# Optimization experiments

Hardware: AMD Instinct MI355X
Metric: run time of the kernel (lower is better)

## Reference

```python
import jax, jax.numpy as jnp
import numpy as np

N = 50000      # num nodes
E = 800000     # num edges
F_IN = 100     # input features (ogbn-products)
HID = 128      # hidden_dim (per-head out_channels)
H = 2          # heads
OUT = 47       # num classes
NEG_SLOPE = 0.2


def setup_inputs() -> dict:
    key = jax.random.key(0)
    ks = jax.random.split(key, 14)
    def glorot(k, shape, fan):
        return jax.random.normal(k, shape, jnp.float32) * (1.0 / np.sqrt(fan))
    x = jax.random.normal(ks[0], (N, F_IN), jnp.float32)
    edge_index = jax.random.randint(ks[1], (2, E), 0, N)
    # GAT layer 0: lin_l (= lin_r, shared) weight [H*HID, F_IN], attention vecs [H, HID]
    W0 = glorot(ks[2], (H * HID, F_IN), F_IN)
    b0 = jnp.zeros((H * HID,), jnp.float32)
    attl0 = glorot(ks[3], (H, HID), HID)
    attr0 = glorot(ks[4], (H, HID), HID)
    # GAT layer 1: input dim H*HID
    W1 = glorot(ks[5], (H * HID, H * HID), H * HID)
    b1 = jnp.zeros((H * HID,), jnp.float32)
    attl1 = glorot(ks[6], (H, HID), HID)
    attr1 = glorot(ks[7], (H, HID), HID)
    # post_mp: Linear(H*HID -> HID), Linear(HID -> OUT)
    Wp1 = glorot(ks[8], (HID, H * HID), H * HID)
    bp1 = jnp.zeros((HID,), jnp.float32)
    Wp2 = glorot(ks[9], (OUT, HID), HID)
    bp2 = jnp.zeros((OUT,), jnp.float32)
    return dict(x=x, edge_index=edge_index, W0=W0, b0=b0, attl0=attl0, attr0=attr0,
                W1=W1, b1=b1, attl1=attl1, attr1=attr1,
                Wp1=Wp1, bp1=bp1, Wp2=Wp2, bp2=bp2)


def gat_layer(x, W, b, att_l, att_r, src, dst):
    # shared lin_l == lin_r in the source
    h = (x @ W.T + b).reshape(-1, H, HID)          # [N, H, C]
    alpha_l = jnp.einsum('nhc,hc->nh', h, att_l)   # per-node left scores
    alpha_r = jnp.einsum('nhc,hc->nh', h, att_r)   # per-node right scores
    e = jax.nn.leaky_relu(alpha_l[src] + alpha_r[dst], NEG_SLOPE)  # [E, H]
    # segment softmax over edges grouped by destination node
    emax = jax.ops.segment_max(e, dst, num_segments=N)             # [N, H]
    ee = jnp.exp(e - emax[dst])
    denom = jax.ops.segment_sum(ee, dst, num_segments=N)           # [N, H]
    a = ee / denom[dst]                                            # [E, H]
    msg = a[:, :, None] * h[src]                                   # [E, H, C]
    out = jax.ops.segment_sum(msg, dst, num_segments=N)            # [N, H, C]
    return out.reshape(-1, H * HID)


def reference(x, edge_index, W0, b0, attl0, attr0, W1, b1, attl1, attr1, Wp1, bp1, Wp2, bp2):
    src, dst = edge_index[0], edge_index[1]
    x = jax.nn.relu(gat_layer(x, W0, b0, attl0, attr0, src, dst))
    x = jax.nn.relu(gat_layer(x, W1, b1, attl1, attr1, src, dst))
    h = x @ Wp1.T + bp1           # dropout p=0.0 -> identity
    logits = h @ Wp2.T + bp2
    return jax.nn.log_softmax(logits, axis=1)
```

## Files before the change

### kernel.cpp

```cpp
#include <hip/hip_runtime.h>
#include <math.h>

#define N_NODES 50000
#define E_EDGES 800000
#define F_IN 100
#define HID 128
#define HEADS 2
#define OUT_C 47
#define HH (HEADS*HID)
#define MPAD 50048
#define SLOTS 64

typedef float floatx4 __attribute__((ext_vector_type(4)));
typedef float float2v __attribute__((ext_vector_type(2)));
typedef short short8 __attribute__((ext_vector_type(8)));

__device__ inline ushort bf16round(float v) {
    unsigned u = __float_as_uint(v);
    return (ushort)((u + 0x7FFFu + ((u >> 16) & 1u)) >> 16);
}

__device__ __forceinline__ void gl_lds16(const void* g, void* l) {
    __builtin_amdgcn_global_load_lds(
        (const __attribute__((address_space(1))) unsigned int*)g,
        (__attribute__((address_space(3))) unsigned int*)l, 16, 0, 0);
}

__device__ __forceinline__ void gemm_body(
    int bx, int by,
    const ushort* __restrict__ Ab, const ushort* __restrict__ Wb,
    const float* __restrict__ bias,
    ushort* __restrict__ Hb,
    const float* __restrict__ attl, const float* __restrict__ attr,
    float* __restrict__ al, float* __restrict__ ar,
    int M, int Kp, ushort* sA, ushort* sB)
{
    const int t = threadIdx.x;
    const int wave = t >> 6, lane = t & 63;
    const int quad = lane >> 4, l16 = lane & 15;
    const int rl = lane >> 2, seg = lane & 3;
    const int m0 = by * 64, n0 = bx * 128;

    floatx4 acc[8];
#pragma unroll
    for (int j = 0; j < 8; j++) acc[j] = (floatx4)(0.f);

    for (int k0 = 0; k0 < Kp; k0 += 32) {
        {
            size_t gro = (size_t)(m0 + wave * 16 + rl) * Kp + k0 + seg * 8;
            gl_lds16(Ab + gro, sA + (wave * 16) * 32);
        }
#pragma unroll
        for (int j = 0; j < 2; j++) {
            int br = wave * 32 + j * 16;
            size_t gro = (size_t)(n0 + br + rl) * Kp + k0 + seg * 8;
            gl_lds16(Wb + gro, sB + br * 32);
        }
        __syncthreads();

        short8 af = *(const short8*)(sA + (wave * 16 + l16) * 32 + quad * 8);
#pragma unroll
        for (int sn = 0; sn < 8; sn++) {
            int r = sn * 16 + l16;
            short8 b = *(const short8*)(sB + r * 32 + quad * 8);
            acc[sn] = __builtin_amdgcn_mfma_f32_16x16x32_bf16(af, b, acc[sn], 0, 0, 0);
        }
        __syncthreads();
    }

    float bias_r[8], att_l[8], att_r[8];
#pragma unroll
    for (int sn = 0; sn < 8; sn++) {
        int ai = n0 + sn * 16 + l16;
        bias_r[sn] = bias[ai];
        att_l[sn] = attl[ai];
        att_r[sn] = attr[ai];
    }
#pragma unroll
    for (int r = 0; r < 4; r++) {
        int gm = m0 + wave * 16 + quad * 4 + r;
        float suml = 0.f, sumr = 0.f;
#pragma unroll
        for (int sn = 0; sn < 8; sn++) {
            float v = acc[sn][r] + bias_r[sn];
            suml += v * att_l[sn];
            sumr += v * att_r[sn];
            if (gm < M) {
                int gn = n0 + sn * 16 + l16;
                Hb[(size_t)gm * 256 + gn] = bf16round(v);
            }
        }
#pragma unroll
        for (int off = 1; off < 16; off <<= 1) {
            suml += __shfl_xor(suml, off);
            sumr += __shfl_xor(sumr, off);
        }
        if (l16 == 0 && gm < M) {
            al[gm * HEADS + bx] = suml;
            ar[gm * HEADS + bx] = sumr;
        }
    }
}

__global__ __launch_bounds__(256) void gemm_l0(
    const ushort* __restrict__ xb, const ushort* __restrict__ W0b,
    const float* __restrict__ b0,
    const float* __restrict__ attl0, const float* __restrict__ attr0,
    ushort* __restrict__ hb, float* __restrict__ al, float* __restrict__ ar)
{
    __shared__ ushort sA[64 * 32], sB[128 * 32];
    gemm_body(blockIdx.x, blockIdx.y, xb, W0b, b0,
              hb, attl0, attr0, al, ar, N_NODES, 128, sA, sB);
}

__global__ __launch_bounds__(256) void gemm_l1(
    const ushort* __restrict__ Ab, const ushort* __restrict__ Wb,
    const float* __restrict__ bias, ushort* __restrict__ Hb,
    const float* __restrict__ attl, const float* __restrict__ attr,
    float* __restrict__ al, float* __restrict__ ar)
{
    __shared__ ushort sA[64 * 32], sB[128 * 32];
    gemm_body(blockIdx.x, blockIdx.y, Ab, Wb, bias,
              Hb, attl, attr, al, ar, N_NODES, HH, sA, sB);
}

__global__ void count_convert(const int* __restrict__ srcv, const int* __restrict__ dstv,
                              int* __restrict__ deg, ushort* __restrict__ csr16,
                              const float* __restrict__ x,  const float* __restrict__ W0,
                              const float* __restrict__ W1, const float* __restrict__ Wp1,
                              const float* __restrict__ Wp2,
                              ushort* __restrict__ xb,  ushort* __restrict__ W0b,
                              ushort* __restrict__ W1b, ushort* __restrict__ Wp1b,
                              ushort* __restrict__ Wp2b) {
    const int cx = N_NODES * 32;
    const int c0 = cx + 256 * 32;
    const int c1 = c0 + (HH * HH) / 4;
    const int c2 = c1 + (HID * HH) / 4;
    const int c3 = c2 + (64 * HID) / 4;
    int i = blockIdx.x * 256 + threadIdx.x;
    if (i < E_EDGES) {
        int d = dstv[i];
        int r = atomicAdd(&deg[d], 1);
        csr16[(size_t)d * SLOTS + r] = (ushort)srcv[i];
    }
    if (i >= c3) return;
    float4 v = make_float4(0.f, 0.f, 0.f, 0.f);
    ushort* H; size_t o;
    if (i < cx) {
        int row = i >> 5, kc = (i & 31) * 4;
        if (kc < F_IN) v = *(const float4*)(x + (size_t)row * F_IN + kc);
        H = xb; o = (size_t)row * 128 + kc;
    } else if (i < c0) {
        int j = i - cx;
        int row = j >> 5, kc = (j & 31) * 4;
        if (kc < F_IN) v = *(const float4*)(W0 + (size_t)row * F_IN + kc);
        H = W0b; o = (size_t)row * 128 + kc;
    } else if (i < c1) {
        int j = i - c0;
        v = *(const float4*)(W1 + (size_t)j * 4);
        H = W1b; o = (size_t)j * 4;
    } else if (i < c2) {
        int j = i - c1;
        v = *(const float4*)(Wp1 + (size_t)j * 4);
        H = Wp1b; o = (size_t)j * 4;
    } else {
        int j = i - c2;
        int row = j >> 5;
        if (row < OUT_C) v = *(const float4*)(Wp2 + (size_t)j * 4);
        H = Wp2b; o = (size_t)j * 4;
    }
    ushort4 r;
    r.x = bf16round(v.x); r.y = bf16round(v.y);
    r.z = bf16round(v.z); r.w = bf16round(v.w);
    *(ushort4*)(H + o) = r;
}

__global__ __launch_bounds__(256) void gat_aggregate(
    const ushort* __restrict__ hb, const float* __restrict__ al, const float* __restrict__ ar,
    const int* __restrict__ deg, const ushort* __restrict__ csr16,
    ushort* __restrict__ outb)
{
    const int node = blockIdx.x * 4 + (threadIdx.x >> 6);
    const int lane = threadIdx.x & 63;
    if (node >= N_NODES) return;
    const int n = deg[node];
    const int half = lane >> 5;
    const int l32  = lane & 31;
    const int headf = l32 >> 4;
    const float2 ard = ((const float2*)ar)[node];

    float dsum0 = 0.f, dsum1 = 0.f;
    float2v av[4];
#pragma unroll
    for (int j = 0; j < 4; j++) av[j] = (float2v)(0.f);

    int s = 0; float w0 = 0.f, w1 = 0.f;
    if (lane < n) {
        s = (int)csr16[(size_t)node * SLOTS + lane];
        float2 aa = ((const float2*)al)[s];
        float e0 = aa.x + ard.x;
        float e1 = aa.y + ard.y;
        e0 = fmaxf(e0, 0.f) + 0.2f * fminf(e0, 0.f);
        e1 = fmaxf(e1, 0.f) + 0.2f * fminf(e1, 0.f);
        w0 = __expf(e0); w1 = __expf(e1);
        dsum0 += w0; dsum1 += w1;
    }
    for (int i = 0; i < n; i += 4) {
        int e0i = i + half;
        int   se0 = __shfl(s,  e0i);
        float u00 = __shfl(w0, e0i);
        float u01 = __shfl(w1, e0i);
        float2v we0 = (float2v)(headf ? u01 : u00);
        const uint4 q0 = *(const uint4*)(hb + (size_t)se0 * 256 + l32 * 8);
        int e1i = i + 2 + half;
        int   se1 = __shfl(s,  e1i);
        float u10 = __shfl(w0, e1i);
        float u11 = __shfl(w1, e1i);
        float2v we1 = (float2v)(headf ? u11 : u10);
        const uint4 q1 = *(const uint4*)(hb + (size_t)se1 * 256 + l32 * 8);
        float2v p;
        p.x = __uint_as_float(q0.x << 16); p.y = __uint_as_float(q0.x & 0xFFFF0000u);
        av[0] += we0 * p;
        p.x = __uint_as_float(q0.y << 16); p.y = __uint_as_float(q0.y & 0xFFFF0000u);
        av[1] += we0 * p;
        p.x = __uint_as_float(q0.z << 16); p.y = __uint_as_float(q0.z & 0xFFFF0000u);
        av[2] += we0 * p;
        p.x = __uint_as_float(q0.w << 16); p.y = __uint_as_float(q0.w & 0xFFFF0000u);
        av[3] += we0 * p;
        p.x = __uint_as_float(q1.x << 16); p.y = __uint_as_float(q1.x & 0xFFFF0000u);
        av[0] += we1 * p;
        p.x = __uint_as_float(q1.y << 16); p.y = __uint_as_float(q1.y & 0xFFFF0000u);
        av[1] += we1 * p;
        p.x = __uint_as_float(q1.z << 16); p.y = __uint_as_float(q1.z & 0xFFFF0000u);
        av[2] += we1 * p;
        p.x = __uint_as_float(q1.w << 16); p.y = __uint_as_float(q1.w & 0xFFFF0000u);
        av[3] += we1 * p;
    }
#pragma unroll
    for (int j = 0; j < 4; j++) {
        av[j].x += __shfl_xor(av[j].x, 32);
        av[j].y += __shfl_xor(av[j].y, 32);
    }
#pragma unroll
    for (int off = 32; off; off >>= 1) {
        dsum0 += __shfl_xor(dsum0, off);
        dsum1 += __shfl_xor(dsum1, off);
    }
    if (half == 0) {
        const float den = headf ? dsum1 : dsum0;
        const float inv = (n > 0) ? 1.f / den : 0.f;
        ushort r[8];
#pragma unroll
        for (int j = 0; j < 4; j++) {
            r[2*j]   = bf16round(fmaxf(av[j].x * inv, 0.f));
            r[2*j+1] = bf16round(fmaxf(av[j].y * inv, 0.f));
        }
        *(uint4*)(outb + (size_t)node * 256 + l32 * 8) = *(uint4*)r;
    }
}

__global__ __launch_bounds__(256) void fused_post(
    const ushort* __restrict__ Ab,
    const ushort* __restrict__ Bb,
    const float* __restrict__ bp1,
    const ushort* __restrict__ W2b,
    const float* __restrict__ bp2,
    float* __restrict__ out, int M)
{
    __shared__ ushort sA[128 * 32];
    __shared__ ushort sB[128 * 32];
    __shared__ ushort sP[128 * 136];

    const int t = threadIdx.x;
    const int wave = t >> 6, lane = t & 63;
    const int quad = lane >> 4, l16 = lane & 15;
    const int rl = lane >> 2, seg = lane & 3;
    const int m0 = blockIdx.x * 128;

    floatx4 acc[2][8];
#pragma unroll
    for (int i = 0; i < 2; i++)
#pragma unroll
        for (int j = 0; j < 8; j++) acc[i][j] = (floatx4)(0.f);

    for (int k0 = 0; k0 < HH; k0 += 32) {
#pragma unroll
        for (int j = 0; j < 2; j++) {
            int br = wave * 32 + j * 16;
            size_t gro = (size_t)(m0 + br + rl) * HH + k0 + seg * 8;
            gl_lds16(Ab + gro, sA + br * 32);
        }
#pragma unroll
        for (int j = 0; j < 2; j++) {
            int br = wave * 32 + j * 16;
            size_t gro = (size_t)(br + rl) * HH + k0 + seg * 8;
            gl_lds16(Bb + gro, sB + br * 32);
        }
        __syncthreads();
        short8 af[2];
#pragma unroll
        for (int sm = 0; sm < 2; sm++) {
            int r = wave * 32 + sm * 16 + l16;
            af[sm] = *(const short8*)(sA + r * 32 + quad * 8);
        }
#pragma unroll
        for (int sn = 0; sn < 8; sn++) {
            int r = sn * 16 + l16;
            short8 b = *(const short8*)(sB + r * 32 + quad * 8);
#pragma unroll
            for (int sm = 0; sm < 2; sm++)
                acc[sm][sn] = __builtin_amdgcn_mfma_f32_16x16x32_bf16(af[sm], b, acc[sm][sn], 0, 0, 0);
        }
        __syncthreads();
    }
#pragma unroll
    for (int sm = 0; sm < 2; sm++)
#pragma unroll
        for (int sn = 0; sn < 8; sn++)
#pragma unroll
            for (int r = 0; r < 4; r++) {
                int row = wave * 32 + sm * 16 + quad * 4 + r;
                int col = sn * 16 + l16;
                sP[row * 136 + col] = bf16round(acc[sm][sn][r] + bp1[col]);
            }
    __syncthreads();

    floatx4 acc2[2][4];
#pragma unroll
    for (int i = 0; i < 2; i++)
#pragma unroll
        for (int j = 0; j < 4; j++) acc2[i][j] = (floatx4)(0.f);

    for (int k0 = 0; k0 < HID; k0 += 32) {
        {
            int br = wave * 16;
            size_t gro = (size_t)(br + rl) * HID + k0 + seg * 8;
            gl_lds16(W2b + gro, sA + br * 32);
        }
        __syncthreads();
        short8 ph[2];
#pragma unroll
        for (int sm = 0; sm < 2; sm++) {
            int r = wave * 32 + sm * 16 + l16;
            ph[sm] = *(const short8*)(sP + r * 136 + k0 + quad * 8);
        }
#pragma unroll
        for (int sn = 0; sn < 4; sn++) {
            int r = sn * 16 + l16;
            short8 b = *(const short8*)(sA + r * 32 + quad * 8);
#pragma unroll
            for (int sm = 0; sm < 2; sm++)
                acc2[sm][sn] = __builtin_amdgcn_mfma_f32_16x16x32_bf16(ph[sm], b, acc2[sm][sn], 0, 0, 0);
        }
        __syncthreads();
    }

    float b2[4];
#pragma unroll
    for (int sn = 0; sn < 4; sn++) {
        int n = sn * 16 + l16;
        b2[sn] = (n < OUT_C) ? bp2[n] : 0.f;
    }
#pragma unroll
    for (int sm = 0; sm < 2; sm++)
#pragma unroll
        for (int r = 0; r < 4; r++) {
            float v[4];
            float m = -INFINITY;
#pragma unroll
            for (int sn = 0; sn < 4; sn++) {
                int n = sn * 16 + l16;
                float xv = (n < OUT_C) ? acc2[sm][sn][r] + b2[sn] : -INFINITY;
                v[sn] = xv;
                m = fmaxf(m, xv);
            }
#pragma unroll
            for (int off = 1; off < 16; off <<= 1) m = fmaxf(m, __shfl_xor(m, off));
            float ssum = 0.f;
#pragma unroll
            for (int sn = 0; sn < 4; sn++) {
                int n = sn * 16 + l16;
                if (n < OUT_C) ssum += __expf(v[sn] - m);
            }
#pragma unroll
            for (int off = 1; off < 16; off <<= 1) ssum += __shfl_xor(ssum, off);
            float lse = m + logf(ssum);
            int gm = m0 + wave * 32 + sm * 16 + quad * 4 + r;
            if (gm < M) {
#pragma unroll
                for (int sn = 0; sn < 4; sn++) {
                    int n = sn * 16 + l16;
                    if (n < OUT_C) out[(size_t)gm * OUT_C + n] = v[sn] - lse;
                }
            }
        }
}

extern "C" void kernel_launch(void* const* d_in, const int* in_sizes, int n_in,
                              void* d_out, int out_size, void* d_ws, size_t ws_size,
                              hipStream_t stream) {
    const float* x     = (const float*)d_in[0];
    const int*   ei    = (const int*)d_in[1];
    const float* W0    = (const float*)d_in[2];
    const float* b0    = (const float*)d_in[3];
    const float* attl0 = (const float*)d_in[4];
    const float* attr0 = (const float*)d_in[5];
    const float* W1    = (const float*)d_in[6];
    const float* b1    = (const float*)d_in[7];
    const float* attl1 = (const float*)d_in[8];
    const float* attr1 = (const float*)d_in[9];
    const float* Wp1   = (const float*)d_in[10];
    const float* bp1   = (const float*)d_in[11];
    const float* Wp2   = (const float*)d_in[12];
    const float* bp2   = (const float*)d_in[13];
    float* out = (float*)d_out;

    const int Nn = N_NODES, Etot = E_EDGES;
    const int* srcv = ei;
    const int* dstv = ei + Etot;

    char* ws = (char*)d_ws;
    size_t off = 0;
    auto alloc = [&](size_t bytes) -> void* {
        void* p = ws + off;
        off = (off + bytes + 255) & ~(size_t)255;
        return p;
    };
    int*    deg    = (int*)alloc((size_t)Nn * sizeof(int));
    ushort* csr16  = (ushort*)alloc((size_t)Nn * SLOTS * 2);
    float*  al     = (float*)alloc((size_t)Nn * HEADS * sizeof(float));
    float*  ar     = (float*)alloc((size_t)Nn * HEADS * sizeof(float));
    ushort* xb     = (ushort*)alloc((size_t)MPAD * 128 * 2);
    ushort* W0b    = (ushort*)alloc((size_t)HH * 128 * 2);
    ushort* W1b    = (ushort*)alloc((size_t)HH * HH * 2);
    ushort* Wp1b   = (ushort*)alloc((size_t)HID * HH * 2);
    ushort* Wp2b   = (ushort*)alloc((size_t)64 * HID * 2);
    ushort* hb     = (ushort*)alloc((size_t)Nn * HH * 2);
    ushort* xbb    = (ushort*)alloc((size_t)MPAD * HH * 2);

    hipMemsetAsync(deg, 0, (size_t)Nn * sizeof(int), stream);

    {
        const int tot = N_NODES * 32 + 256 * 32 + (HH * HH) / 4 + (HID * HH) / 4 + (64 * HID) / 4;
        const int grid = (tot + 255) / 256;
        count_convert<<<grid, 256, 0, stream>>>(
            srcv, dstv, deg, csr16, x, W0, W1, Wp1, Wp2, xb, W0b, W1b, Wp1b, Wp2b);
    }

    {
        dim3 g(2, MPAD / 64);
        gemm_l0<<<g, 256, 0, stream>>>(xb, W0b, b0, attl0, attr0, hb, al, ar);
    }

    gat_aggregate<<<(Nn + 3) / 4, 256, 0, stream>>>(hb, al, ar, deg, csr16, xbb);

    {
        dim3 g(2, MPAD / 64);
        gemm_l1<<<g, 256, 0, stream>>>(xbb, W1b, b1, hb, attl1, attr1, al, ar);
    }
    gat_aggregate<<<(Nn + 3) / 4, 256, 0, stream>>>(hb, al, ar, deg, csr16, xbb);

    fused_post<<<MPAD / 128, 256, 0, stream>>>(xbb, Wp1b, bp1, Wp2b, bp2, out, Nn);
}
```

Measured before the change: 299.2 us.

## Split aggregation by head and map heads to XCDs for L2 locality

The aggregation kernel now handles one head per wave instead of both. Block index bits route each head to a fixed set of XCDs (even or odd), so each XCD's L2 only caches half of the feature rows. Each wave gathers 8 edges per iteration using 16-lane groups with 16-byte loads. The cost is twice as many blocks, so softmax scores and CSR indices are loaded twice, and there is an extra cross-lane reduction step.

```diff
diff --git a/kernel.cpp b/kernel.cpp
--- a/kernel.cpp
+++ b/kernel.cpp
@@ -180,44 +180,44 @@
     const int* __restrict__ deg, const ushort* __restrict__ csr16,
     ushort* __restrict__ outb)
 {
-    const int node = blockIdx.x * 4 + (threadIdx.x >> 6);
+    const int g = blockIdx.x;
+    const int xcd = g & 7;
+    const int head = xcd & 1;
+    const int rank = (g >> 3) * 4 + (xcd >> 1);
+    const int wave = threadIdx.x >> 6;
+    const int node = rank * 4 + wave;
     const int lane = threadIdx.x & 63;
+    const int grp = lane >> 4, c = lane & 15;
     if (node >= N_NODES) return;
     const int n = deg[node];
-    const int half = lane >> 5;
-    const int l32  = lane & 31;
-    const int headf = l32 >> 4;
-    const float2 ard = ((const float2*)ar)[node];
-
-    float dsum0 = 0.f, dsum1 = 0.f;
+    const float ard = ar[node * HEADS + head];
+    const ushort* __restrict__ hbh = hb + head * HID + c * 8;
+
+    float dsum = 0.f;
     float2v av[4];
 #pragma unroll
     for (int j = 0; j < 4; j++) av[j] = (float2v)(0.f);
 
-    int s = 0; float w0 = 0.f, w1 = 0.f;
+    int s = 0; float w = 0.f;
     if (lane < n) {
         s = (int)csr16[(size_t)node * SLOTS + lane];
-        float2 aa = ((const float2*)al)[s];
-        float e0 = aa.x + ard.x;
-        float e1 = aa.y + ard.y;
-        e0 = fmaxf(e0, 0.f) + 0.2f * fminf(e0, 0.f);
-        e1 = fmaxf(e1, 0.f) + 0.2f * fminf(e1, 0.f);
-        w0 = __expf(e0); w1 = __expf(e1);
-        dsum0 += w0; dsum1 += w1;
-    }
-    for (int i = 0; i < n; i += 4) {
-        int e0i = i + half;
-        int   se0 = __shfl(s,  e0i);
-        float u00 = __shfl(w0, e0i);
-        float u01 = __shfl(w1, e0i);
-        float2v we0 = (float2v)(headf ? u01 : u00);
-        const uint4 q0 = *(const uint4*)(hb + (size_t)se0 * 256 + l32 * 8);
-        int e1i = i + 2 + half;
-        int   se1 = __shfl(s,  e1i);
-        float u10 = __shfl(w0, e1i);
-        float u11 = __shfl(w1, e1i);
-        float2v we1 = (float2v)(headf ? u11 : u10);
-        const uint4 q1 = *(const uint4*)(hb + (size_t)se1 * 256 + l32 * 8);
+        float e = al[s * HEADS + head] + ard;
+        e = fmaxf(e, 0.f) + 0.2f * fminf(e, 0.f);
+        w = __expf(e);
+        dsum = w;
+    }
+    for (int i = 0; i < n; i += 8) {
+        int e0 = i + grp, e1 = i + 4 + grp;
+        int   s0 = __shfl(s, e0);
+        float w0 = __shfl(w, e0);
+        int   s1 = __shfl(s, e1);
+        float w1 = __shfl(w, e1);
+        uint4 q0 = make_uint4(0u, 0u, 0u, 0u);
+        uint4 q1 = make_uint4(0u, 0u, 0u, 0u);
+        if (e0 < n) q0 = *(const uint4*)(hbh + (size_t)s0 * 256);
+        if (e1 < n) q1 = *(const uint4*)(hbh + (size_t)s1 * 256);
+        float2v we0 = (float2v)(w0);
+        float2v we1 = (float2v)(w1);
         float2v p;
         p.x = __uint_as_float(q0.x << 16); p.y = __uint_as_float(q0.x & 0xFFFF0000u);
         av[0] += we0 * p;
@@ -238,24 +238,23 @@
     }
 #pragma unroll
     for (int j = 0; j < 4; j++) {
+        av[j].x += __shfl_xor(av[j].x, 16);
+        av[j].y += __shfl_xor(av[j].y, 16);
         av[j].x += __shfl_xor(av[j].x, 32);
         av[j].y += __shfl_xor(av[j].y, 32);
     }
 #pragma unroll
-    for (int off = 32; off; off >>= 1) {
-        dsum0 += __shfl_xor(dsum0, off);
-        dsum1 += __shfl_xor(dsum1, off);
-    }
-    if (half == 0) {
-        const float den = headf ? dsum1 : dsum0;
-        const float inv = (n > 0) ? 1.f / den : 0.f;
+    for (int off = 32; off; off >>= 1) dsum += __shfl_xor(dsum, off);
+
+    if (grp == 0) {
+        const float inv = (n > 0) ? 1.f / dsum : 0.f;
         ushort r[8];
 #pragma unroll
         for (int j = 0; j < 4; j++) {
             r[2*j]   = bf16round(fmaxf(av[j].x * inv, 0.f));
             r[2*j+1] = bf16round(fmaxf(av[j].y * inv, 0.f));
         }
-        *(uint4*)(outb + (size_t)node * 256 + l32 * 8) = *(uint4*)r;
+        *(uint4*)(outb + (size_t)node * 256 + head * HID + c * 8) = *(uint4*)r;
     }
 }
 
@@ -452,13 +451,13 @@
         gemm_l0<<<g, 256, 0, stream>>>(xb, W0b, b0, attl0, attr0, hb, al, ar);
     }
 
-    gat_aggregate<<<(Nn + 3) / 4, 256, 0, stream>>>(hb, al, ar, deg, csr16, xbb);
+    gat_aggregate<<<25000, 256, 0, stream>>>(hb, al, ar, deg, csr16, xbb);
 
     {
         dim3 g(2, MPAD / 64);
         gemm_l1<<<g, 256, 0, stream>>>(xbb, W1b, b1, hb, attl1, attr1, al, ar);
     }
-    gat_aggregate<<<(Nn + 3) / 4, 256, 0, stream>>>(hb, al, ar, deg, csr16, xbb);
+    gat_aggregate<<<25000, 256, 0, stream>>>(hb, al, ar, deg, csr16, xbb);
 
     fused_post<<<MPAD / 128, 256, 0, stream>>>(xbb, Wp1b, bp1, Wp2b, bp2, out, Nn);
 }
```

Result: no change. 297.3 us (-0.7%).

## Fuse GAT aggregation into following GEMMs via LDS-staged aggregated rows

Applied to the files above, without the earlier changes.

Each aggregation pass now writes its aggregated, ReLU'd bf16 rows straight into LDS, and the next GEMM consumes them from there. The first fused kernel covers layer-1 aggregation plus the layer-2 linear and attention scores. The second covers layer-2 aggregation plus the post-MP MLP and log-softmax. This removes the intermediate xbb round trip through global memory and two kernel launches. In exchange, each block computes the full 256-wide N tile with 64 rows and one wave serially aggregates 16 nodes, so occupancy drops and the GEMM cannot start until aggregation finishes within the block.

```diff
diff --git a/kernel.cpp b/kernel.cpp
--- a/kernel.cpp
+++ b/kernel.cpp
@@ -10,6 +10,7 @@
 #define HH (HEADS*HID)
 #define MPAD 50048
 #define SLOTS 64
+#define APAD 264
 
 typedef float floatx4 __attribute__((ext_vector_type(4)));
 typedef float float2v __attribute__((ext_vector_type(2)));
@@ -26,168 +27,18 @@
         (__attribute__((address_space(3))) unsigned int*)l, 16, 0, 0);
 }
 
-__device__ __forceinline__ void gemm_body(
-    int bx, int by,
-    const ushort* __restrict__ Ab, const ushort* __restrict__ Wb,
-    const float* __restrict__ bias,
-    ushort* __restrict__ Hb,
-    const float* __restrict__ attl, const float* __restrict__ attr,
-    float* __restrict__ al, float* __restrict__ ar,
-    int M, int Kp, ushort* sA, ushort* sB)
+__device__ __forceinline__ void agg_node_to_lds(
+    int node, int lane,
+    const ushort* __restrict__ hb, const float* __restrict__ al,
+    const float* __restrict__ ar, const int* __restrict__ deg,
+    const ushort* __restrict__ csr16, ushort* dstRow)
 {
-    const int t = threadIdx.x;
-    const int wave = t >> 6, lane = t & 63;
-    const int quad = lane >> 4, l16 = lane & 15;
-    const int rl = lane >> 2, seg = lane & 3;
-    const int m0 = by * 64, n0 = bx * 128;
-
-    floatx4 acc[8];
-#pragma unroll
-    for (int j = 0; j < 8; j++) acc[j] = (floatx4)(0.f);
-
-    for (int k0 = 0; k0 < Kp; k0 += 32) {
-        {
-            size_t gro = (size_t)(m0 + wave * 16 + rl) * Kp + k0 + seg * 8;
-            gl_lds16(Ab + gro, sA + (wave * 16) * 32);
-        }
-#pragma unroll
-        for (int j = 0; j < 2; j++) {
-            int br = wave * 32 + j * 16;
-            size_t gro = (size_t)(n0 + br + rl) * Kp + k0 + seg * 8;
-            gl_lds16(Wb + gro, sB + br * 32);
-        }
-        __syncthreads();
-
-        short8 af = *(const short8*)(sA + (wave * 16 + l16) * 32 + quad * 8);
-#pragma unroll
-        for (int sn = 0; sn < 8; sn++) {
-            int r = sn * 16 + l16;
-            short8 b = *(const short8*)(sB + r * 32 + quad * 8);
-            acc[sn] = __builtin_amdgcn_mfma_f32_16x16x32_bf16(af, b, acc[sn], 0, 0, 0);
-        }
-        __syncthreads();
-    }
-
-    float bias_r[8], att_l[8], att_r[8];
-#pragma unroll
-    for (int sn = 0; sn < 8; sn++) {
-        int ai = n0 + sn * 16 + l16;
-        bias_r[sn] = bias[ai];
-        att_l[sn] = attl[ai];
-        att_r[sn] = attr[ai];
-    }
-#pragma unroll
-    for (int r = 0; r < 4; r++) {
-        int gm = m0 + wave * 16 + quad * 4 + r;
-        float suml = 0.f, sumr = 0.f;
-#pragma unroll
-        for (int sn = 0; sn < 8; sn++) {
-            float v = acc[sn][r] + bias_r[sn];
-            suml += v * att_l[sn];
-            sumr += v * att_r[sn];
-            if (gm < M) {
-                int gn = n0 + sn * 16 + l16;
-                Hb[(size_t)gm * 256 + gn] = bf16round(v);
-            }
-        }
-#pragma unroll
-        for (int off = 1; off < 16; off <<= 1) {
-            suml += __shfl_xor(suml, off);
-            sumr += __shfl_xor(sumr, off);
-        }
-        if (l16 == 0 && gm < M) {
-            al[gm * HEADS + bx] = suml;
-            ar[gm * HEADS + bx] = sumr;
-        }
-    }
-}
-
-__global__ __launch_bounds__(256) void gemm_l0(
-    const ushort* __restrict__ xb, const ushort* __restrict__ W0b,
-    const float* __restrict__ b0,
-    const float* __restrict__ attl0, const float* __restrict__ attr0,
-    ushort* __restrict__ hb, float* __restrict__ al, float* __restrict__ ar)
-{
-    __shared__ ushort sA[64 * 32], sB[128 * 32];
-    gemm_body(blockIdx.x, blockIdx.y, xb, W0b, b0,
-              hb, attl0, attr0, al, ar, N_NODES, 128, sA, sB);
-}
-
-__global__ __launch_bounds__(256) void gemm_l1(
-    const ushort* __restrict__ Ab, const ushort* __restrict__ Wb,
-    const float* __restrict__ bias, ushort* __restrict__ Hb,
-    const float* __restrict__ attl, const float* __restrict__ attr,
-    float* __restrict__ al, float* __restrict__ ar)
-{
-    __shared__ ushort sA[64 * 32], sB[128 * 32];
-    gemm_body(blockIdx.x, blockIdx.y, Ab, Wb, bias,
-              Hb, attl, attr, al, ar, N_NODES, HH, sA, sB);
-}
-
-__global__ void count_convert(const int* __restrict__ srcv, const int* __restrict__ dstv,
-                              int* __restrict__ deg, ushort* __restrict__ csr16,
-                              const float* __restrict__ x,  const float* __restrict__ W0,
-                              const float* __restrict__ W1, const float* __restrict__ Wp1,
-                              const float* __restrict__ Wp2,
-                              ushort* __restrict__ xb,  ushort* __restrict__ W0b,
-                              ushort* __restrict__ W1b, ushort* __restrict__ Wp1b,
-                              ushort* __restrict__ Wp2b) {
-    const int cx = N_NODES * 32;
-    const int c0 = cx + 256 * 32;
-    const int c1 = c0 + (HH * HH) / 4;
-    const int c2 = c1 + (HID * HH) / 4;
-    const int c3 = c2 + (64 * HID) / 4;
-    int i = blockIdx.x * 256 + threadIdx.x;
-    if (i < E_EDGES) {
-        int d = dstv[i];
-        int r = atomicAdd(&deg[d], 1);
-        csr16[(size_t)d * SLOTS + r] = (ushort)srcv[i];
-    }
-    if (i >= c3) return;
-    float4 v = make_float4(0.f, 0.f, 0.f, 0.f);
-    ushort* H; size_t o;
-    if (i < cx) {
-        int row = i >> 5, kc = (i & 31) * 4;
-        if (kc < F_IN) v = *(const float4*)(x + (size_t)row * F_IN + kc);
-        H = xb; o = (size_t)row * 128 + kc;
-    } else if (i < c0) {
-        int j = i - cx;
-        int row = j >> 5, kc = (j & 31) * 4;
-        if (kc < F_IN) v = *(const float4*)(W0 + (size_t)row * F_IN + kc);
-        H = W0b; o = (size_t)row * 128 + kc;
-    } else if (i < c1) {
-        int j = i - c0;
-        v = *(const float4*)(W1 + (size_t)j * 4);
-        H = W1b; o = (size_t)j * 4;
-    } else if (i < c2) {
-        int j = i - c1;
-        v = *(const float4*)(Wp1 + (size_t)j * 4);
-        H = Wp1b; o = (size_t)j * 4;
-    } else {
-        int j = i - c2;
-        int row = j >> 5;
-        if (row < OUT_C) v = *(const float4*)(Wp2 + (size_t)j * 4);
-        H = Wp2b; o = (size_t)j * 4;
-    }
-    ushort4 r;
-    r.x = bf16round(v.x); r.y = bf16round(v.y);
-    r.z = bf16round(v.z); r.w = bf16round(v.w);
-    *(ushort4*)(H + o) = r;
-}
-
-__global__ __launch_bounds__(256) void gat_aggregate(
-    const ushort* __restrict__ hb, const float* __restrict__ al, const float* __restrict__ ar,
-    const int* __restrict__ deg, const ushort* __restrict__ csr16,
-    ushort* __restrict__ outb)
-{
-    const int node = blockIdx.x * 4 + (threadIdx.x >> 6);
-    const int lane = threadIdx.x & 63;
-    if (node >= N_NODES) return;
-    const int n = deg[node];
     const int half = lane >> 5;
     const int l32  = lane & 31;
     const int headf = l32 >> 4;
-    const float2 ard = ((const float2*)ar)[node];
+    const int n = (node < N_NODES) ? deg[node] : 0;
+    float2 ard = make_float2(0.f, 0.f);
+    if (node < N_NODES) ard = ((const float2*)ar)[node];
 
     float dsum0 = 0.f, dsum1 = 0.f;
     float2v av[4];
@@ -255,41 +106,212 @@
             r[2*j]   = bf16round(fmaxf(av[j].x * inv, 0.f));
             r[2*j+1] = bf16round(fmaxf(av[j].y * inv, 0.f));
         }
-        *(uint4*)(outb + (size_t)node * 256 + l32 * 8) = *(uint4*)r;
-    }
-}
-
-__global__ __launch_bounds__(256) void fused_post(
-    const ushort* __restrict__ Ab,
+        *(uint4*)(dstRow + l32 * 8) = *(uint4*)r;
+    }
+}
+
+__device__ __forceinline__ void gemm_body(
+    int bx, int by,
+    const ushort* __restrict__ Ab, const ushort* __restrict__ Wb,
+    const float* __restrict__ bias,
+    ushort* __restrict__ Hb,
+    const float* __restrict__ attl, const float* __restrict__ attr,
+    float* __restrict__ al, float* __restrict__ ar,
+    int M, int Kp, ushort* sA, ushort* sB)
+{
+    const int t = threadIdx.x;
+    const int wave = t >> 6, lane = t & 63;
+    const int quad = lane >> 4, l16 = lane & 15;
+    const int rl = lane >> 2, seg = lane & 3;
+    const int m0 = by * 64, n0 = bx * 128;
+
+    floatx4 acc[8];
+#pragma unroll
+    for (int j = 0; j < 8; j++) acc[j] = (floatx4)(0.f);
+
+    for (int k0 = 0; k0 < Kp; k0 += 32) {
+        {
+            size_t gro = (size_t)(m0 + wave * 16 + rl) * Kp + k0 + seg * 8;
+            gl_lds16(Ab + gro, sA + (wave * 16) * 32);
+        }
+#pragma unroll
+        for (int j = 0; j < 2; j++) {
+            int br = wave * 32 + j * 16;
+            size_t gro = (size_t)(n0 + br + rl) * Kp + k0 + seg * 8;
+            gl_lds16(Wb + gro, sB + br * 32);
+        }
+        __syncthreads();
+
+        short8 af = *(const short8*)(sA + (wave * 16 + l16) * 32 + quad * 8);
+#pragma unroll
+        for (int sn = 0; sn < 8; sn++) {
+            int r = sn * 16 + l16;
+            short8 b = *(const short8*)(sB + r * 32 + quad * 8);
+            acc[sn] = __builtin_amdgcn_mfma_f32_16x16x32_bf16(af, b, acc[sn], 0, 0, 0);
+        }
+        __syncthreads();
+    }
+
+    float bias_r[8], att_l[8], att_r[8];
+#pragma unroll
+    for (int sn = 0; sn < 8; sn++) {
+        int ai = n0 + sn * 16 + l16;
+        bias_r[sn] = bias[ai];
+        att_l[sn] = attl[ai];
+        att_r[sn] = attr[ai];
+    }
+#pragma unroll
+    for (int r = 0; r < 4; r++) {
+        int gm = m0 + wave * 16 + quad * 4 + r;
+        float suml = 0.f, sumr = 0.f;
+#pragma unroll
+        for (int sn = 0; sn < 8; sn++) {
+            float v = acc[sn][r] + bias_r[sn];
+            suml += v * att_l[sn];
+            sumr += v * att_r[sn];
+            if (gm < M) {
+                int gn = n0 + sn * 16 + l16;
+                Hb[(size_t)gm * 256 + gn] = bf16round(v);
+            }
+        }
+#pragma unroll
+        for (int off = 1; off < 16; off <<= 1) {
+            suml += __shfl_xor(suml, off);
+            sumr += __shfl_xor(sumr, off);
+        }
+        if (l16 == 0 && gm < M) {
+            al[gm * HEADS + bx] = suml;
+            ar[gm * HEADS + bx] = sumr;
+        }
+    }
+}
+
+__global__ __launch_bounds__(256) void gemm_l0(
+    const ushort* __restrict__ xb, const ushort* __restrict__ W0b,
+    const float* __restrict__ b0,
+    const float* __restrict__ attl0, const float* __restrict__ attr0,
+    ushort* __restrict__ hb, float* __restrict__ al, float* __restrict__ ar)
+{
+    __shared__ ushort sA[64 * 32], sB[128 * 32];
+    gemm_body(blockIdx.x, blockIdx.y, xb, W0b, b0,
+              hb, attl0, attr0, al, ar, N_NODES, 128, sA, sB);
+}
+
+__global__ __launch_bounds__(256) void fused_agg_gemm(
+    const ushort* __restrict__ hb, const float* __restrict__ al,
+    const float* __restrict__ ar, const int* __restrict__ deg,
+    const ushort* __restrict__ csr16,
+    const ushort* __restrict__ Wb,
+    const float* __restrict__ bias,
+    const float* __restrict__ attl, const float* __restrict__ attr,
+    ushort* __restrict__ Hb2, float* __restrict__ al2, float* __restrict__ ar2)
+{
+    __shared__ ushort sA[64 * APAD];
+    __shared__ ushort sB[256 * 32];
+
+    const int t = threadIdx.x;
+    const int wave = t >> 6, lane = t & 63;
+    const int quad = lane >> 4, l16 = lane & 15;
+    const int rl = lane >> 2, seg = lane & 3;
+    const int m0 = blockIdx.x * 64;
+
+    for (int j = 0; j < 16; j++) {
+        int node = m0 + wave * 16 + j;
+        agg_node_to_lds(node, lane, hb, al, ar, deg, csr16,
+                        sA + (size_t)(wave * 16 + j) * APAD);
+    }
+    __syncthreads();
+
+    floatx4 acc[16];
+#pragma unroll
+    for (int j = 0; j < 16; j++) acc[j] = (floatx4)(0.f);
+
+    for (int k0 = 0; k0 < HH; k0 += 32) {
+#pragma unroll
+        for (int j = 0; j < 4; j++) {
+            int br = wave * 64 + j * 16;
+            size_t gro = (size_t)(br + rl) * HH + k0 + seg * 8;
+            gl_lds16(Wb + gro, sB + br * 32);
+        }
+        __syncthreads();
+        short8 af = *(const short8*)(sA + (wave * 16 + l16) * APAD + k0 + quad * 8);
+#pragma unroll
+        for (int sn = 0; sn < 16; sn++) {
+            short8 b = *(const short8*)(sB + (sn * 16 + l16) * 32 + quad * 8);
+            acc[sn] = __builtin_amdgcn_mfma_f32_16x16x32_bf16(af, b, acc[sn], 0, 0, 0);
+        }
+        __syncthreads();
+    }
+
+#pragma unroll
+    for (int h = 0; h < 2; h++) {
+        float bias_r[8], att_l[8], att_r[8];
+#pragma unroll
+        for (int sn = 0; sn < 8; sn++) {
+            int ai = h * 128 + sn * 16 + l16;
+            bias_r[sn] = bias[ai];
+            att_l[sn] = attl[ai];
+            att_r[sn] = attr[ai];
+        }
+#pragma unroll
+        for (int r = 0; r < 4; r++) {
+            int gm = m0 + wave * 16 + quad * 4 + r;
+            float suml = 0.f, sumr = 0.f;
+#pragma unroll
+            for (int sn = 0; sn < 8; sn++) {
+                float v = acc[h * 8 + sn][r] + bias_r[sn];
+                suml += v * att_l[sn];
+                sumr += v * att_r[sn];
+                if (gm < N_NODES) {
+                    int gn = h * 128 + sn * 16 + l16;
+                    Hb2[(size_t)gm * 256 + gn] = bf16round(v);
+                }
+            }
+#pragma unroll
+            for (int off = 1; off < 16; off <<= 1) {
+                suml += __shfl_xor(suml, off);
+                sumr += __shfl_xor(sumr, off);
+            }
+            if (l16 == 0 && gm < N_NODES) {
+                al2[gm * HEADS + h] = suml;
+                ar2[gm * HEADS + h] = sumr;
+            }
+        }
+    }
+}
+
+__global__ __launch_bounds__(256) void fused_agg_post(
+    const ushort* __restrict__ hb2, const float* __restrict__ al2,
+    const float* __restrict__ ar2, const int* __restrict__ deg,
+    const ushort* __restrict__ csr16,
     const ushort* __restrict__ Bb,
     const float* __restrict__ bp1,
     const ushort* __restrict__ W2b,
     const float* __restrict__ bp2,
     float* __restrict__ out, int M)
 {
-    __shared__ ushort sA[128 * 32];
+    __shared__ ushort sA[64 * APAD];
     __shared__ ushort sB[128 * 32];
-    __shared__ ushort sP[128 * 136];
+    __shared__ ushort sP[64 * 136];
 
     const int t = threadIdx.x;
     const int wave = t >> 6, lane = t & 63;
     const int quad = lane >> 4, l16 = lane & 15;
     const int rl = lane >> 2, seg = lane & 3;
-    const int m0 = blockIdx.x * 128;
-
-    floatx4 acc[2][8];
-#pragma unroll
-    for (int i = 0; i < 2; i++)
-#pragma unroll
-        for (int j = 0; j < 8; j++) acc[i][j] = (floatx4)(0.f);
+    const int m0 = blockIdx.x * 64;
+
+    for (int j = 0; j < 16; j++) {
+        int node = m0 + wave * 16 + j;
+        agg_node_to_lds(node, lane, hb2, al2, ar2, deg, csr16,
+                        sA + (size_t)(wave * 16 + j) * APAD);
+    }
+    __syncthreads();
+
+    floatx4 acc[8];
+#pragma unroll
+    for (int j = 0; j < 8; j++) acc[j] = (floatx4)(0.f);
 
     for (int k0 = 0; k0 < HH; k0 += 32) {
-#pragma unroll
-        for (int j = 0; j < 2; j++) {
-            int br = wave * 32 + j * 16;
-            size_t gro = (size_t)(m0 + br + rl) * HH + k0 + seg * 8;
-            gl_lds16(Ab + gro, sA + br * 32);
-        }
 #pragma unroll
         for (int j = 0; j < 2; j++) {
             int br = wave * 32 + j * 16;
@@ -297,60 +319,40 @@
             gl_lds16(Bb + gro, sB + br * 32);
         }
         __syncthreads();
-        short8 af[2];
-#pragma unroll
-        for (int sm = 0; sm < 2; sm++) {
-            int r = wave * 32 + sm * 16 + l16;
-            af[sm] = *(const short8*)(sA + r * 32 + quad * 8);
-        }
+        short8 af = *(const short8*)(sA + (wave * 16 + l16) * APAD + k0 + quad * 8);
 #pragma unroll
         for (int sn = 0; sn < 8; sn++) {
-            int r = sn * 16 + l16;
-            short8 b = *(const short8*)(sB + r * 32 + quad * 8);
-#pragma unroll
-            for (int sm = 0; sm < 2; sm++)
-                acc[sm][sn] = __builtin_amdgcn_mfma_f32_16x16x32_bf16(af[sm], b, acc[sm][sn], 0, 0, 0);
-        }
-        __syncthreads();
-    }
-#pragma unroll
-    for (int sm = 0; sm < 2; sm++)
-#pragma unroll
-        for (int sn = 0; sn < 8; sn++)
-#pragma unroll
-            for (int r = 0; r < 4; r++) {
-                int row = wave * 32 + sm * 16 + quad * 4 + r;
-                int col = sn * 16 + l16;
-                sP[row * 136 + col] = bf16round(acc[sm][sn][r] + bp1[col]);
-            }
+            short8 b = *(const short8*)(sB + (sn * 16 + l16) * 32 + quad * 8);
+            acc[sn] = __builtin_amdgcn_mfma_f32_16x16x32_bf16(af, b, acc[sn], 0, 0, 0);
+        }
+        __syncthreads();
+    }
+#pragma unroll
+    for (int sn = 0; sn < 8; sn++)
+#pragma unroll
+        for (int r = 0; r < 4; r++) {
+            int row = wave * 16 + quad * 4 + r;
+            int col = sn * 16 + l16;
+            sP[row * 136 + col] = bf16round(acc[sn][r] + bp1[col]);
+        }
     __syncthreads();
 
-    floatx4 acc2[2][4];
-#pragma unroll
-    for (int i = 0; i < 2; i++)
-#pragma unroll
-        for (int j = 0; j < 4; j++) acc2[i][j] = (floatx4)(0.f);
+    floatx4 acc2[4];
+#pragma unroll
+    for (int j = 0; j < 4; j++) acc2[j] = (floatx4)(0.f);
 
     for (int k0 = 0; k0 < HID; k0 += 32) {
         {
             int br = wave * 16;
             size_t gro = (size_t)(br + rl) * HID + k0 + seg * 8;
-            gl_lds16(W2b + gro, sA + br * 32);
-        }
-        __syncthreads();
-        short8 ph[2];
-#pragma unroll
-        for (int sm = 0; sm < 2; sm++) {
-            int r = wave * 32 + sm * 16 + l16;
-            ph[sm] = *(const short8*)(sP + r * 136 + k0 + quad * 8);
-        }
+            gl_lds16(W2b + gro, sB + br * 32);
+        }
+        __syncthreads();
+        short8 ph = *(const short8*)(sP + (wave * 16 + l16) * 136 + k0 + quad * 8);
 #pragma unroll
         for (int sn = 0; sn < 4; sn++) {
-            int r = sn * 16 + l16;
-            short8 b = *(const short8*)(sA + r * 32 + quad * 8);
-#pragma unroll
-            for (int sm = 0; sm < 2; sm++)
-                acc2[sm][sn] = __builtin_amdgcn_mfma_f32_16x16x32_bf16(ph[sm], b, acc2[sm][sn], 0, 0, 0);
+            short8 b = *(const short8*)(sB + (sn * 16 + l16) * 32 + quad * 8);
+            acc2[sn] = __builtin_amdgcn_mfma_f32_16x16x32_bf16(ph, b, acc2[sn], 0, 0, 0);
         }
         __syncthreads();
     }
@@ -362,38 +364,87 @@
         b2[sn] = (n < OUT_C) ? bp2[n] : 0.f;
     }
 #pragma unroll
-    for (int sm = 0; sm < 2; sm++)
-#pragma unroll
-        for (int r = 0; r < 4; r++) {
-            float v[4];
-            float m = -INFINITY;
+    for (int r = 0; r < 4; r++) {
+        float v[4];
+        float m = -INFINITY;
+#pragma unroll
+        for (int sn = 0; sn < 4; sn++) {
+            int n = sn * 16 + l16;
+            float xv = (n < OUT_C) ? acc2[sn][r] + b2[sn] : -INFINITY;
+            v[sn] = xv;
+            m = fmaxf(m, xv);
+        }
+#pragma unroll
+        for (int off = 1; off < 16; off <<= 1) m = fmaxf(m, __shfl_xor(m, off));
+        float ssum = 0.f;
+#pragma unroll
+        for (int sn = 0; sn < 4; sn++) {
+            int n = sn * 16 + l16;
+            if (n < OUT_C) ssum += __expf(v[sn] - m);
+        }
+#pragma unroll
+        for (int off = 1; off < 16; off <<= 1) ssum += __shfl_xor(ssum, off);
+        float lse = m + logf(ssum);
+        int gm = m0 + wave * 16 + quad * 4 + r;
+        if (gm < M) {
 #pragma unroll
             for (int sn = 0; sn < 4; sn++) {
                 int n = sn * 16 + l16;
-                float xv = (n < OUT_C) ? acc2[sm][sn][r] + b2[sn] : -INFINITY;
-                v[sn] = xv;
-                m = fmaxf(m, xv);
+                if (n < OUT_C) out[(size_t)gm * OUT_C + n] = v[sn] - lse;
             }
-#pragma unroll
-            for (int off = 1; off < 16; off <<= 1) m = fmaxf(m, __shfl_xor(m, off));
-            float ssum = 0.f;
-#pragma unroll
-            for (int sn = 0; sn < 4; sn++) {
-                int n = sn * 16 + l16;
-                if (n < OUT_C) ssum += __expf(v[sn] - m);
-            }
-#pragma unroll
-            for (int off = 1; off < 16; off <<= 1) ssum += __shfl_xor(ssum, off);
-            float lse = m + logf(ssum);
-            int gm = m0 + wave * 32 + sm * 16 + quad * 4 + r;
-            if (gm < M) {
-#pragma unroll
-                for (int sn = 0; sn < 4; sn++) {
-                    int n = sn * 16 + l16;
-                    if (n < OUT_C) out[(size_t)gm * OUT_C + n] = v[sn] - lse;
-                }
-            }
-        }
+        }
+    }
+}
+
+__global__ void count_convert(const int* __restrict__ srcv, const int* __restrict__ dstv,
+                              int* __restrict__ deg, ushort* __restrict__ csr16,
+                              const float* __restrict__ x,  const float* __restrict__ W0,
+                              const float* __restrict__ W1, const float* __restrict__ Wp1,
+                              const float* __restrict__ Wp2,
+                              ushort* __restrict__ xb,  ushort* __restrict__ W0b,
+                              ushort* __restrict__ W1b, ushort* __restrict__ Wp1b,
+                              ushort* __restrict__ Wp2b) {
+    const int cx = N_NODES * 32;
+    const int c0 = cx + 256 * 32;
+    const int c1 = c0 + (HH * HH) / 4;
+    const int c2 = c1 + (HID * HH) / 4;
+    const int c3 = c2 + (64 * HID) / 4;
+    int i = blockIdx.x * 256 + threadIdx.x;
+    if (i < E_EDGES) {
+        int d = dstv[i];
+        int r = atomicAdd(&deg[d], 1);
+        csr16[(size_t)d * SLOTS + r] = (ushort)srcv[i];
+    }
+    if (i >= c3) return;
+    float4 v = make_float4(0.f, 0.f, 0.f, 0.f);
+    ushort* H; size_t o;
+    if (i < cx) {
+        int row = i >> 5, kc = (i & 31) * 4;
+        if (kc < F_IN) v = *(const float4*)(x + (size_t)row * F_IN + kc);
+        H = xb; o = (size_t)row * 128 + kc;
+    } else if (i < c0) {
+        int j = i - cx;
+        int row = j >> 5, kc = (j & 31) * 4;
+        if (kc < F_IN) v = *(const float4*)(W0 + (size_t)row * F_IN + kc);
+        H = W0b; o = (size_t)row * 128 + kc;
+    } else if (i < c1) {
+        int j = i - c0;
+        v = *(const float4*)(W1 + (size_t)j * 4);
+        H = W1b; o = (size_t)j * 4;
+    } else if (i < c2) {
+        int j = i - c1;
+        v = *(const float4*)(Wp1 + (size_t)j * 4);
+        H = Wp1b; o = (size_t)j * 4;
+    } else {
+        int j = i - c2;
+        int row = j >> 5;
+        if (row < OUT_C) v = *(const float4*)(Wp2 + (size_t)j * 4);
+        H = Wp2b; o = (size_t)j * 4;
+    }
+    ushort4 r;
+    r.x = bf16round(v.x); r.y = bf16round(v.y);
+    r.z = bf16round(v.z); r.w = bf16round(v.w);
+    *(ushort4*)(H + o) = r;
 }
 
 extern "C" void kernel_launch(void* const* d_in, const int* in_sizes, int n_in,
@@ -430,13 +481,15 @@
     ushort* csr16  = (ushort*)alloc((size_t)Nn * SLOTS * 2);
     float*  al     = (float*)alloc((size_t)Nn * HEADS * sizeof(float));
     float*  ar     = (float*)alloc((size_t)Nn * HEADS * sizeof(float));
+    float*  al2    = (float*)alloc((size_t)Nn * HEADS * sizeof(float));
+    float*  ar2    = (float*)alloc((size_t)Nn * HEADS * sizeof(float));
     ushort* xb     = (ushort*)alloc((size_t)MPAD * 128 * 2);
     ushort* W0b    = (ushort*)alloc((size_t)HH * 128 * 2);
     ushort* W1b    = (ushort*)alloc((size_t)HH * HH * 2);
     ushort* Wp1b   = (ushort*)alloc((size_t)HID * HH * 2);
     ushort* Wp2b   = (ushort*)alloc((size_t)64 * HID * 2);
     ushort* hb     = (ushort*)alloc((size_t)Nn * HH * 2);
-    ushort* xbb    = (ushort*)alloc((size_t)MPAD * HH * 2);
+    ushort* hb2    = (ushort*)alloc((size_t)Nn * HH * 2);
 
     hipMemsetAsync(deg, 0, (size_t)Nn * sizeof(int), stream);
 
@@ -452,13 +505,9 @@
         gemm_l0<<<g, 256, 0, stream>>>(xb, W0b, b0, attl0, attr0, hb, al, ar);
     }
 
-    gat_aggregate<<<(Nn + 3) / 4, 256, 0, stream>>>(hb, al, ar, deg, csr16, xbb);
-
-    {
-        dim3 g(2, MPAD / 64);
-        gemm_l1<<<g, 256, 0, stream>>>(xbb, W1b, b1, hb, attl1, attr1, al, ar);
-    }
-    gat_aggregate<<<(Nn + 3) / 4, 256, 0, stream>>>(hb, al, ar, deg, csr16, xbb);
-
-    fused_post<<<MPAD / 128, 256, 0, stream>>>(xbb, Wp1b, bp1, Wp2b, bp2, out, Nn);
-}
+    fused_agg_gemm<<<MPAD / 64, 256, 0, stream>>>(
+        hb, al, ar, deg, csr16, W1b, b1, attl1, attr1, hb2, al2, ar2);
+
+    fused_agg_post<<<MPAD / 64, 256, 0, stream>>>(
+        hb2, al2, ar2, deg, csr16, Wp1b, bp1, Wp2b, bp2, out, Nn);
+}
```

After: 395.9 us. 1.32x slower.
